# Performance work log

Measured on AMD Instinct MI355X. Metric: run time of the kernel, lower is better.

## Reference

```python
import jax, jax.numpy as jnp
import numpy as np


def _lstm(x, h0, c0, Wih, Whh, b):
    """Single-layer LSTM, batch_first input x: [B,T,D]. PyTorch gate order i,f,g,o.
    Returns (h_seq [T,B,H], h_T [B,H], c_T [B,H])."""
    xs = jnp.swapaxes(x, 0, 1)  # [T,B,D]

    def step(carry, xt):
        h, c = carry
        gates = xt @ Wih.T + h @ Whh.T + b  # [B,4H]
        i, f, g, o = jnp.split(gates, 4, axis=-1)
        c = jax.nn.sigmoid(f) * c + jax.nn.sigmoid(i) * jnp.tanh(g)
        h = jax.nn.sigmoid(o) * jnp.tanh(c)
        return (h, c), h

    (h, c), hs = jax.lax.scan(step, (h0, c0), xs)
    return hs, h, c


def setup_inputs() -> dict:
    key = jax.random.key(0)
    ks = jax.random.split(key, 16)
    B, T, Tf, Tu = 256, 365, 15, 76
    Dh, Df, Du, H = 64, 32, 16, 256
    s = 1.0 / np.sqrt(H)  # torch-style uniform scale, approximated with scaled normals
    return {
        "x_d": jax.random.normal(ks[0], (B, T, Dh), jnp.float32),
        "x_f": jax.random.normal(ks[1], (B, Tf, Df), jnp.float32),
        "x_ff": jax.random.normal(ks[2], (B, Tu, Du), jnp.float32),
        "enc_Wih": jax.random.normal(ks[3], (4 * H, Dh), jnp.float32) * s,
        "enc_Whh": jax.random.normal(ks[4], (4 * H, H), jnp.float32) * s,
        "enc_b": jax.random.normal(ks[5], (4 * H,), jnp.float32) * s,
        "decf_Wih": jax.random.normal(ks[6], (4 * H, Df), jnp.float32) * s,
        "decf_Whh": jax.random.normal(ks[7], (4 * H, H), jnp.float32) * s,
        "decf_b": jax.random.normal(ks[8], (4 * H,), jnp.float32) * s,
        "decu_Wih": jax.random.normal(ks[9], (4 * H, Du), jnp.float32) * s,
        "decu_Whh": jax.random.normal(ks[10], (4 * H, H), jnp.float32) * s,
        "decu_b": jax.random.normal(ks[11], (4 * H,), jnp.float32) * s,
        "head_W": jax.random.normal(ks[12], (1, H), jnp.float32) * s,
        "head_b": jax.random.normal(ks[13], (1,), jnp.float32) * s,
    }


def reference(x_d, x_f, x_ff, enc_Wih, enc_Whh, enc_b,
              decf_Wih, decf_Whh, decf_b, decu_Wih, decu_Whh, decu_b,
              head_W, head_b):
    B = x_d.shape[0]
    H = enc_Whh.shape[1]
    Tf = x_f.shape[1]
    Tu = x_ff.shape[1]
    horizon = Tf + Tu
    h0 = jnp.zeros((B, H), x_d.dtype)
    c0 = jnp.zeros((B, H), x_d.dtype)

    # Encoder over historical sequence
    _, h, c = _lstm(x_d, h0, c0, enc_Wih, enc_Whh, enc_b)

    # Forecast decoder: one LSTM step per horizon step + linear head (dropout = eval identity)
    hs_f, h, c = _lstm(x_f, h, c, decf_Wih, decf_Whh, decf_b)  # [Tf,B,H]
    out_f = (jnp.einsum('tbh,oh->tbo', hs_f, head_W)[..., 0] + head_b[0]).T  # [B,Tf]

    # Future decoder, continuing the hidden state
    hs_u, h, c = _lstm(x_ff, h, c, decu_Wih, decu_Whh, decu_b)  # [Tu,B,H]
    out_u = (jnp.einsum('tbh,oh->tbo', hs_u, head_W)[..., 0] + head_b[0]).T  # [B,Tu]

    # Faithful to original: both loops write outputs[:, t], so the future loop
    # overwrites the first Tu columns.
    outputs = jnp.zeros((B, horizon), x_d.dtype)
    outputs = outputs.at[:, :Tf].set(out_f)
    outputs = outputs.at[:, :Tu].set(out_u)
    return outputs
```

## Files before the change

### kernel.cpp

```cpp
#include <hip/hip_runtime.h>
#include <stdint.h>


typedef __attribute__((ext_vector_type(8))) short short8;
typedef __attribute__((ext_vector_type(4))) float f32x4;
typedef __attribute__((ext_vector_type(2))) unsigned int u32x2;
typedef __attribute__((ext_vector_type(4))) unsigned int u32x4;

#define L2E 1.4426950408889634f

__device__ __forceinline__ uint16_t f2bf(float f) {
  uint32_t x = __float_as_uint(f);
  x += 0x7fffu + ((x >> 16) & 1u);
  return (uint16_t)(x >> 16);
}
__device__ __forceinline__ uint32_t cvtpk(float lo, float hi) {
  uint32_t r;
  asm("v_cvt_pk_bf16_f32 %0, %1, %2" : "=v"(r) : "v"(lo), "v"(hi));
  return r;
}
__device__ __forceinline__ float bfhalf(uint32_t w, int hi) {
  return __uint_as_float(hi ? (w & 0xffff0000u) : (w << 16));
}
__device__ __forceinline__ f32x4 MFMA(short8 a, short8 b, f32x4 c) {
  return __builtin_amdgcn_mfma_f32_16x16x32_bf16(a, b, c, 0, 0, 0);
}
__device__ __forceinline__ float ex2(float x) { return __builtin_amdgcn_exp2f(x); }
__device__ __forceinline__ float rcp(float x) { return __builtin_amdgcn_rcpf(x); }

__device__ __forceinline__ short8 pack8s(const float* s, float sc) {
  float4 q0 = *(const float4*)s, q1 = *(const float4*)(s + 4);
  u32x4 t;
  t[0] = cvtpk(q0.x * sc, q0.y * sc);
  t[1] = cvtpk(q0.z * sc, q0.w * sc);
  t[2] = cvtpk(q1.x * sc, q1.y * sc);
  t[3] = cvtpk(q1.z * sc, q1.w * sc);
  return *(short8*)&t;
}

__device__ __forceinline__ void lgkm_barrier() {
  __builtin_amdgcn_sched_barrier(0);
  asm volatile("s_waitcnt lgkmcnt(0)" ::: "memory");
  __builtin_amdgcn_s_barrier();
  __builtin_amdgcn_sched_barrier(0);
}
__device__ __forceinline__ void vm_drain4() {
  __builtin_amdgcn_sched_barrier(0);
  asm volatile("s_waitcnt vmcnt(4)" ::: "memory");
  __builtin_amdgcn_sched_barrier(0);
}

__global__ void init_kernel(float* c_state, uint16_t* h_state, float* out) {
  int i = blockIdx.x * 256 + threadIdx.x;
  if (i < 65536) { c_state[i] = 0.f; h_state[i] = 0; }
  if (i < 256 * 91) out[i] = 0.f;
}

template <int DIN>
__device__ __forceinline__ void xproj_body(
    const float* __restrict__ x, const float* __restrict__ Wih,
    const float* __restrict__ bias, uint32_t* __restrict__ xp,
    int T, int blk, int tid) {
  const int w = tid >> 6, l = tid & 63;
  const int l16 = l & 15, lg = l >> 4;
  const int tc = blk >> 1;
  const int sub = blk & 1;
  const int t = tc;
  constexpr int KT = (DIN + 31) / 32;

  short8 bfr[8][KT];
  float4 bias4[8];
#pragma unroll
  for (int ni = 0; ni < 8; ++ni) {
    const int n = (w * 8 + ni) * 16 + l16;
    bias4[ni] = *(const float4*)&bias[(w * 8 + ni) * 16 + lg * 4];
#pragma unroll
    for (int kt = 0; kt < KT; ++kt) {
      const int k0 = kt * 32 + lg * 8;
      short8 fr;
#pragma unroll
      for (int e = 0; e < 8; ++e) fr[e] = 0;
      if (k0 + 8 <= DIN) fr = pack8s(Wih + (size_t)n * DIN + k0, 1.f);
      bfr[ni][kt] = fr;
    }
  }

  for (int mi = 0; mi < 8; ++mi) {
    const int btile = sub * 8 + mi;
    const int b = btile * 16 + l16;
    short8 af[KT];
#pragma unroll
    for (int kt = 0; kt < KT; ++kt) {
      const int k0 = kt * 32 + lg * 8;
      short8 fr;
#pragma unroll
      for (int e = 0; e < 8; ++e) fr[e] = 0;
      if (k0 + 8 <= DIN) fr = pack8s(x + ((size_t)b * T + t) * DIN + k0, 1.f);
      af[kt] = fr;
    }
#pragma unroll
    for (int ni = 0; ni < 8; ++ni) {
      f32x4 acc = {0.f, 0.f, 0.f, 0.f};
#pragma unroll
      for (int kt = 0; kt < KT; ++kt) acc = MFMA(bfr[ni][kt], af[kt], acc);
      const int nt = w * 8 + ni;
      const float sc = ((nt >> 4) == 2) ? (2.f * L2E) : -L2E;
      size_t idx = ((((size_t)tc * 16 + btile) * 64 + nt) * 64 + l) * 2;
      u32x2 v;
      v[0] = cvtpk((acc[0] + bias4[ni].x) * sc, (acc[1] + bias4[ni].y) * sc);
      v[1] = cvtpk((acc[2] + bias4[ni].z) * sc, (acc[3] + bias4[ni].w) * sc);
      *(u32x2*)(xp + idx) = v;
    }
  }
}

template <int DIN>
__global__ __launch_bounds__(512) void xproj_kernel(
    const float* __restrict__ x, const float* __restrict__ Wih,
    const float* __restrict__ bias, uint32_t* __restrict__ xp,
    int t0, int T) {
  const int tid = threadIdx.x;
  const int blk = blockIdx.x + t0 * 2;
  xproj_body<DIN>(x, Wih, bias, xp - (size_t)t0 * 131072, T, blk, tid);
}

__global__ __launch_bounds__(512) void xproj_mega(
    const float* __restrict__ x0, const float* __restrict__ Wih0,
    const float* __restrict__ b0, uint32_t* __restrict__ xp0,
    const float* __restrict__ x1, const float* __restrict__ Wih1,
    const float* __restrict__ b1, uint32_t* __restrict__ xp1,
    const float* __restrict__ x2, const float* __restrict__ Wih2,
    const float* __restrict__ b2, uint32_t* __restrict__ xp2,
    float* __restrict__ out, uint32_t* __restrict__ flags,
    int T0, int T1, int T2) {
  const int tid = threadIdx.x;
  const int n0 = T0 * 2, n1 = T1 * 2, n2 = T2 * 2;
  const int b = blockIdx.x;
  if (b < n0) {
    xproj_body<64>(x0, Wih0, b0, xp0, T0, b, tid);
  } else if (b < n0 + n1) {
    xproj_body<32>(x1, Wih1, b1, xp1, T1, b - n0, tid);
  } else if (b < n0 + n1 + n2) {
    xproj_body<16>(x2, Wih2, b2, xp2, T2, b - n0 - n1, tid);
  } else {
    for (int i = tid; i < 256 * 15; i += 512)
      out[(size_t)(i / 15) * 91 + 76 + (i % 15)] = 0.f;
    if (tid < 96) flags[tid] = 0;
  }
}

template <int DO_HEAD, int ZINIT>
__global__ __launch_bounds__(512, 2) void rec_kernel(
    const uint32_t* __restrict__ xp, const float* __restrict__ Whh,
    float* __restrict__ c_state, uint16_t* __restrict__ h_state,
    float* __restrict__ out, const float* __restrict__ headW,
    const float* __restrict__ headb, int ct, int tcol0) {
  __shared__ short8 B_lds[8 * 16 * 64];
  __shared__ uint16_t h_lds[2][16][264];
  __shared__ float headbuf[2][16][8];

  const int tid = threadIdx.x, w = tid >> 6, l = tid & 63;
  const int l16 = l & 15, lg = l >> 4;
  const int blk = blockIdx.x, b0 = blk * 16;

  short8 bv[48];
#pragma unroll
  for (int g = 0; g < 4; ++g) {
    const float wsc = (g == 2) ? (2.f * L2E) : -L2E;
#pragma unroll
    for (int nt = 0; nt < 2; ++nt)
#pragma unroll
      for (int kt = 0; kt < 8; ++kt) {
        const int row = (g * 16 + w * 2 + nt) * 16 + l16;
        const float* s = Whh + (size_t)row * 256 + kt * 32 + lg * 8;
        short8 fr;
#pragma unroll
        for (int e = 0; e < 8; ++e) fr[e] = (short)f2bf(s[e] * wsc);
        const int tile = g * 2 + nt;
        if (kt <= 5) bv[tile * 6 + kt] = fr;
        else B_lds[(w * 16 + (kt - 6) * 8 + tile) * 64 + l] = fr;
      }
  }

  float c_reg[2][4];
  if (ZINIT) {
#pragma unroll
    for (int nt = 0; nt < 2; ++nt)
#pragma unroll
      for (int j = 0; j < 4; ++j) c_reg[nt][j] = 0.f;
    for (int idx = tid; idx < 16 * 264; idx += 512)
      ((uint16_t*)h_lds)[idx] = 0;
  } else {
#pragma unroll
    for (int nt = 0; nt < 2; ++nt) {
      float4 c4 = *(const float4*)&c_state[(size_t)(b0 + l16) * 256 +
                                           (w * 2 + nt) * 16 + lg * 4];
      c_reg[nt][0] = c4.x; c_reg[nt][1] = c4.y;
      c_reg[nt][2] = c4.z; c_reg[nt][3] = c4.w;
    }
    for (int idx = tid; idx < 16 * 256; idx += 512)
      h_lds[0][idx >> 8][idx & 255] = h_state[(size_t)(b0 + (idx >> 8)) * 256 + (idx & 255)];
  }
  float4 hw4[2];
#pragma unroll
  for (int nt = 0; nt < 2; ++nt)
    hw4[nt] = *(const float4*)&headW[(w * 2 + nt) * 16 + lg * 4];
  const float hb = headb[0];

  const uint32_t* xpb = xp + ((size_t)(blk * 64 + w * 2) * 64 + l) * 2;
  u32x2 xpf[2][4];
#pragma unroll
  for (int nt = 0; nt < 2; ++nt)
#pragma unroll
    for (int g = 0; g < 4; ++g)
      xpf[nt][g] = *(const u32x2*)(xpb + (size_t)g * 2048 + nt * 128);

  __syncthreads();

  for (int t = 0; t < ct; ++t) {
    const int cur = t & 1, nxt = cur ^ 1;
    const int tn = (t + 1 < ct) ? t + 1 : t;
    float hp = 0.f;

#pragma unroll
    for (int nt = 0; nt < 2; ++nt) {
      f32x4 acc[4];
#pragma unroll
      for (int g = 0; g < 4; ++g) {
        f32x4 ai;
        ai[0] = bfhalf(xpf[nt][g][0], 0);
        ai[1] = bfhalf(xpf[nt][g][0], 1);
        ai[2] = bfhalf(xpf[nt][g][1], 0);
        ai[3] = bfhalf(xpf[nt][g][1], 1);
        acc[g] = ai;
      }
#pragma unroll
      for (int kt = 0; kt <= 5; ++kt) {
        short8 hf = *(const short8*)(&h_lds[cur][l16][kt * 32 + lg * 8]);
#pragma unroll
        for (int g = 0; g < 4; ++g)
          acc[g] = MFMA(bv[(g * 2 + nt) * 6 + kt], hf, acc[g]);
      }
#pragma unroll
      for (int kt = 6; kt <= 7; ++kt) {
        short8 hf = *(const short8*)(&h_lds[cur][l16][kt * 32 + lg * 8]);
#pragma unroll
        for (int g = 0; g < 4; ++g)
          acc[g] = MFMA(B_lds[(w * 16 + (kt - 6) * 8 + g * 2 + nt) * 64 + l], hf, acc[g]);
      }

      float hv[4];
#pragma unroll
      for (int j = 0; j < 4; ++j) {
        float ei = ex2(acc[0][j]);
        float ef = ex2(acc[1][j]);
        float eg = ex2(acc[2][j]);
        float eo = ex2(acc[3][j]);
        float eip = 1.f + ei, egp = eg + 1.f, efp = 1.f + ef;
        float d1 = eip * egp;
        float R = rcp(d1 * efp);
        float sitg = (eg - 1.f) * efp * R;
        float cc = fmaf(c_reg[nt][j] * d1, R, sitg);
        c_reg[nt][j] = cc;
        float ec = ex2(cc * (2.f * L2E));
        float hh = (ec - 1.f) * rcp((1.f + eo) * (ec + 1.f));
        hv[j] = hh;
      }
      if (DO_HEAD) {
        hp = fmaf(hv[0], hw4[nt].x, hp); hp = fmaf(hv[1], hw4[nt].y, hp);
        hp = fmaf(hv[2], hw4[nt].z, hp); hp = fmaf(hv[3], hw4[nt].w, hp);
      }
      {
        u32x2 hwrd;
        hwrd[0] = cvtpk(hv[0], hv[1]);
        hwrd[1] = cvtpk(hv[2], hv[3]);
        *(u32x2*)(&h_lds[nxt][l16][(w * 2 + nt) * 16 + lg * 4]) = hwrd;
      }
#pragma unroll
      for (int g = 0; g < 4; ++g)
        xpf[nt][g] = *(const u32x2*)(xpb + (size_t)tn * 131072 + g * 2048 + nt * 128);
    }

    if (DO_HEAD) {
      float s = hp;
      s += __shfl_xor(s, 16);
      s += __shfl_xor(s, 32);
      if (lg == 0) headbuf[t & 1][l16][w] = s;
    }

    lgkm_barrier();

    if (DO_HEAD) {
      if (tid < 16) {
        const float* hbp = headbuf[t & 1][tid];
        float s = hbp[0] + hbp[1] + hbp[2] + hbp[3] + hbp[4] + hbp[5] + hbp[6] + hbp[7];
        out[(size_t)(b0 + tid) * 91 + (tcol0 + t)] = s + hb;
      }
    }
  }

#pragma unroll
  for (int nt = 0; nt < 2; ++nt) {
    float4 c4 = {c_reg[nt][0], c_reg[nt][1], c_reg[nt][2], c_reg[nt][3]};
    *(float4*)&c_state[(size_t)(b0 + l16) * 256 + (w * 2 + nt) * 16 + lg * 4] = c4;
  }
  for (int idx = tid; idx < 16 * 256; idx += 512)
    h_state[(size_t)(b0 + (idx >> 8)) * 256 + (idx & 255)] = h_lds[ct & 1][idx >> 8][idx & 255];
}

__global__ __launch_bounds__(512, 2) void rec_split2(
    const uint32_t* __restrict__ xp1g, const uint32_t* __restrict__ xp2g,
    const float* __restrict__ Whh1, const float* __restrict__ Whh2,
    const float* __restrict__ c_state, const uint16_t* __restrict__ h_state,
    float* __restrict__ out, const float* __restrict__ headW,
    const float* __restrict__ headb, uint32_t* __restrict__ flags,
    unsigned long long* __restrict__ hx, uint32_t* __restrict__ hxh,
    int T1, int T2) {
  __shared__ short8 B_lds[64 * 64];
  __shared__ uint16_t h_lds[2][16][264];
  __shared__ float headbuf[16][8];

  const int tid = threadIdx.x, w = tid >> 6, l = tid & 63;
  const int l16 = l & 15, lg = l >> 4;
  const int blk = blockIdx.x;
  const int pair = blk & 15, s = blk >> 4, sp = 1 - s;
  const int b0 = pair * 16;
  const int ctile = s * 8 + w;

  float c_reg[4];
  {
    float4 c4 = *(const float4*)&c_state[(size_t)(b0 + l16) * 256 +
                                         ctile * 16 + lg * 4];
    c_reg[0] = c4.x; c_reg[1] = c4.y; c_reg[2] = c4.z; c_reg[3] = c4.w;
  }
  for (int idx = tid; idx < 16 * 256; idx += 512)
    h_lds[0][idx >> 8][idx & 255] = h_state[(size_t)(b0 + (idx >> 8)) * 256 + (idx & 255)];
  float4 hw4 = *(const float4*)&headW[ctile * 16 + lg * 4];
  const float hb = headb[0];

  float hsum_prev = 0.f;

#pragma unroll
  for (int p = 0; p < 2; ++p) {
    const float* Whh = p ? Whh2 : Whh1;
    const uint32_t* xp = p ? xp2g : xp1g;
    const int ct = p ? T2 : T1;
    const bool headf = (p == 1);
    uint32_t* const pflag = flags + ((1 + p) * 16 + pair) * 2 + sp;
    uint32_t* const myflag = flags + ((1 + p) * 16 + pair) * 2 + s;
    unsigned long long* const hxp = hx + (size_t)p * 32768;
    uint32_t* const hxhp = hxh + p * 1024;

    short8 bv[24];
#pragma unroll
    for (int g = 0; g < 4; ++g) {
      const float wsc = (g == 2) ? (2.f * L2E) : -L2E;
#pragma unroll
      for (int kk = 0; kk < 8; ++kk) {
        const int kt = (kk < 4) ? (4 * s + kk) : (4 * sp + (kk - 4));
        const int row = (g * 16 + ctile) * 16 + l16;
        const float* sw = Whh + (size_t)row * 256 + kt * 32 + lg * 8;
        short8 fr;
#pragma unroll
        for (int e = 0; e < 8; ++e) fr[e] = (short)f2bf(sw[e] * wsc);
        if (kk <= 5) bv[g * 6 + kk] = fr;
        else B_lds[(w * 8 + g * 2 + (kk - 6)) * 64 + l] = fr;
      }
    }

    const uint32_t* xpb = xp + ((size_t)(pair * 64 + ctile) * 64 + l) * 2;
    u32x2 xpf[4];
#pragma unroll
    for (int g = 0; g < 4; ++g)
      xpf[g] = *(const u32x2*)(xpb + (size_t)g * 2048);

    __syncthreads();

    u32x2 h_last; h_last[0] = 0; h_last[1] = 0;

    for (int t = 0; t < ct; ++t) {
      const int cur = t & 1, nxt = cur ^ 1;
      const int tn = (t + 1 < ct) ? t + 1 : t;
      const int par = t & 1;

      unsigned long long pv = 0ull;
      if (t > 0) {
        const uint32_t tgt = (uint32_t)t;
        __builtin_amdgcn_sched_barrier(0);
        uint32_t f;
        do {
          f = __hip_atomic_load(pflag, __ATOMIC_RELAXED, __HIP_MEMORY_SCOPE_AGENT);
        } while ((int)(f - tgt) < 0);
        __builtin_amdgcn_sched_barrier(0);
        pv = __hip_atomic_load(
            hxp + ((size_t)((pair * 2 + sp) * 2 + ((t - 1) & 1)) * 512) +
                (w * 4 + lg) * 16 + l16,
            __ATOMIC_RELAXED, __HIP_MEMORY_SCOPE_AGENT);
        if (headf && s == 0 && tid < 16) {
          uint32_t pp = __hip_atomic_load(
              hxhp + ((pair * 2 + sp) * 2 + ((t - 1) & 1)) * 16 + tid,
              __ATOMIC_RELAXED, __HIP_MEMORY_SCOPE_AGENT);
          out[(size_t)(b0 + tid) * 91 + (t - 1)] =
              hsum_prev + __uint_as_float(pp) + hb;
        }
      }

      f32x4 acc[4];
#pragma unroll
      for (int g = 0; g < 4; ++g) {
        f32x4 ai;
        ai[0] = bfhalf(xpf[g][0], 0);
        ai[1] = bfhalf(xpf[g][0], 1);
        ai[2] = bfhalf(xpf[g][1], 0);
        ai[3] = bfhalf(xpf[g][1], 1);
        acc[g] = ai;
      }
#pragma unroll
      for (int kk = 0; kk < 4; ++kk) {
        short8 hf = *(const short8*)(&h_lds[cur][l16][(4 * s + kk) * 32 + lg * 8]);
#pragma unroll
        for (int g = 0; g < 4; ++g)
          acc[g] = MFMA(bv[g * 6 + kk], hf, acc[g]);
      }

      if (t > 0) {
        u32x2 pw;
        pw[0] = (uint32_t)pv;
        pw[1] = (uint32_t)(pv >> 32);
        *(u32x2*)(&h_lds[cur][l16][sp * 128 + w * 16 + lg * 4]) = pw;
        lgkm_barrier();
      }

#pragma unroll
      for (int kk = 0; kk < 4; ++kk) {
        short8 hf = *(const short8*)(&h_lds[cur][l16][(4 * sp + kk) * 32 + lg * 8]);
#pragma unroll
        for (int g = 0; g < 4; ++g) {
          if (kk < 2) acc[g] = MFMA(bv[g * 6 + 4 + kk], hf, acc[g]);
          else acc[g] = MFMA(B_lds[(w * 8 + g * 2 + (kk - 2)) * 64 + l], hf, acc[g]);
        }
      }

      float hv[4];
#pragma unroll
      for (int j = 0; j < 4; ++j) {
        float ei = ex2(acc[0][j]);
        float ef = ex2(acc[1][j]);
        float eg = ex2(acc[2][j]);
        float eo = ex2(acc[3][j]);
        float eip = 1.f + ei, egp = eg + 1.f, efp = 1.f + ef;
        float d1 = eip * egp;
        float R = rcp(d1 * efp);
        float sitg = (eg - 1.f) * efp * R;
        float cc = fmaf(c_reg[j] * d1, R, sitg);
        c_reg[j] = cc;
        float ec = ex2(cc * (2.f * L2E));
        float hh = (ec - 1.f) * rcp((1.f + eo) * (ec + 1.f));
        hv[j] = hh;
      }

      h_last[0] = cvtpk(hv[0], hv[1]);
      h_last[1] = cvtpk(hv[2], hv[3]);
      *(u32x2*)(&h_lds[nxt][l16][ctile * 16 + lg * 4]) = h_last;
      {
        unsigned long long v64 =
            ((unsigned long long)h_last[1] << 32) | (unsigned long long)h_last[0];
        __hip_atomic_store(
            hxp + ((size_t)((pair * 2 + s) * 2 + par) * 512) + (w * 4 + lg) * 16 + l16,
            v64, __ATOMIC_RELAXED, __HIP_MEMORY_SCOPE_AGENT);
      }

#pragma unroll
      for (int g = 0; g < 4; ++g)
        xpf[g] = *(const u32x2*)(xpb + (size_t)tn * 131072 + g * 2048);

      if (headf) {
        float hp = fmaf(hv[0], hw4.x, fmaf(hv[1], hw4.y,
                   fmaf(hv[2], hw4.z, hv[3] * hw4.w)));
        hp += __shfl_xor(hp, 16);
        hp += __shfl_xor(hp, 32);
        if (lg == 0) headbuf[l16][w] = hp;
      }

      vm_drain4();
      lgkm_barrier();

      if (headf) {
        if (tid < 16) {
          const float* hbp = headbuf[tid];
          hsum_prev = hbp[0] + hbp[1] + hbp[2] + hbp[3] +
                      hbp[4] + hbp[5] + hbp[6] + hbp[7];
          __hip_atomic_store(hxhp + ((pair * 2 + s) * 2 + par) * 16 + tid,
                             __float_as_uint(hsum_prev), __ATOMIC_RELAXED,
                             __HIP_MEMORY_SCOPE_AGENT);
        }
        vm_drain4();
      }
      if (tid == 0)
        __hip_atomic_store(myflag, (uint32_t)(t + 1), __ATOMIC_RELAXED,
                           __HIP_MEMORY_SCOPE_AGENT);
    }

    if (p == 0) {
      const uint32_t tgt = (uint32_t)ct;
      __builtin_amdgcn_sched_barrier(0);
      uint32_t f;
      do {
        f = __hip_atomic_load(pflag, __ATOMIC_RELAXED, __HIP_MEMORY_SCOPE_AGENT);
      } while ((int)(f - tgt) < 0);
      __builtin_amdgcn_sched_barrier(0);
      unsigned long long pv = __hip_atomic_load(
          hxp + ((size_t)((pair * 2 + sp) * 2 + ((ct - 1) & 1)) * 512) +
              (w * 4 + lg) * 16 + l16,
          __ATOMIC_RELAXED, __HIP_MEMORY_SCOPE_AGENT);
      const int fb = ct & 1;
      u32x2 pw;
      pw[0] = (uint32_t)pv;
      pw[1] = (uint32_t)(pv >> 32);
      *(u32x2*)(&h_lds[fb][l16][sp * 128 + w * 16 + lg * 4]) = pw;
      lgkm_barrier();
      if (fb != 0) {
        for (int idx = tid; idx < 1024; idx += 512) {
          const int r = idx >> 6, c4v = (idx & 63) * 4;
          *(u32x2*)(&h_lds[0][r][c4v]) = *(const u32x2*)(&h_lds[1][r][c4v]);
        }
      }
      lgkm_barrier();
    }
  }

  if (s == 0 && tid < 16) {
    uint32_t* const pflag2 = flags + (2 * 16 + pair) * 2 + sp;
    const uint32_t tgt = (uint32_t)T2;
    uint32_t f;
    do {
      f = __hip_atomic_load(pflag2, __ATOMIC_RELAXED, __HIP_MEMORY_SCOPE_AGENT);
    } while ((int)(f - tgt) < 0);
    uint32_t pp = __hip_atomic_load(
        hxh + 1024 + ((pair * 2 + sp) * 2 + ((T2 - 1) & 1)) * 16 + tid,
        __ATOMIC_RELAXED, __HIP_MEMORY_SCOPE_AGENT);
    out[(size_t)(b0 + tid) * 91 + (T2 - 1)] =
        hsum_prev + __uint_as_float(pp) + hb;
  }
}

extern "C" void kernel_launch(void* const* d_in, const int* in_sizes, int n_in,
                              void* d_out, int out_size, void* d_ws, size_t ws_size,
                              hipStream_t stream) {
  const float* headW = (const float*)d_in[12];
  const float* headb = (const float*)d_in[13];
  float* out = (float*)d_out;
  char* ws = (char*)d_ws;

  const int T0 = in_sizes[0] / (256 * 64);
  const int T1 = in_sizes[1] / (256 * 32);
  const int T2 = in_sizes[2] / (256 * 16);
  const size_t s0 = (size_t)T0 << 19, s1 = (size_t)T1 << 19, s2 = (size_t)T2 << 19;
  const size_t hdr = 929792;

  if (ws_size >= hdr + s0 + s1 + s2) {
    float* c_state = (float*)ws;
    uint16_t* h_state = (uint16_t*)(ws + 262144);
    uint32_t* flags = (uint32_t*)(ws + 393216);
    unsigned long long* hx = (unsigned long long*)(ws + 397312);
    uint32_t* hxh = (uint32_t*)(ws + 921600);
    uint32_t* xp0 = (uint32_t*)(ws + hdr);
    uint32_t* xp1 = (uint32_t*)(ws + hdr + s0);
    uint32_t* xp2 = (uint32_t*)(ws + hdr + s0 + s1);

    const int nblk = T0 * 2 + T1 * 2 + T2 * 2 + 1;
    xproj_mega<<<dim3(nblk), 512, 0, stream>>>(
        (const float*)d_in[0], (const float*)d_in[3], (const float*)d_in[5], xp0,
        (const float*)d_in[1], (const float*)d_in[6], (const float*)d_in[8], xp1,
        (const float*)d_in[2], (const float*)d_in[9], (const float*)d_in[11], xp2,
        out, flags, T0, T1, T2);
    rec_kernel<0, 1><<<16, 512, 0, stream>>>(xp0, (const float*)d_in[4], c_state,
                                             h_state, out, headW, headb, T0, 0);
    rec_split2<<<32, 512, 0, stream>>>(xp1, xp2, (const float*)d_in[7],
                                       (const float*)d_in[10], c_state, h_state,
                                       out, headW, headb, flags, hx, hxh, T1, T2);
    return;
  }

  float* c_state = (float*)ws;
  uint16_t* h_state = (uint16_t*)(ws + 262144);
  uint32_t* xp = (uint32_t*)(ws + 393216);

  int ct_max = 1;
  if (ws_size > 393216 + 512 * 1024) {
    size_t c = (ws_size - 393216) / (512 * 1024);
    ct_max = (c > 365) ? 365 : (int)c;
  }

  init_kernel<<<256, 256, 0, stream>>>(c_state, h_state, out);

  struct Phase { const float* x; const float* Wih; const float* Whh; const float* b; int T; int D; int head; };
  Phase ph[3] = {
      {(const float*)d_in[0], (const float*)d_in[3], (const float*)d_in[4], (const float*)d_in[5], T0, 64, 0},
      {(const float*)d_in[1], (const float*)d_in[6], (const float*)d_in[7], (const float*)d_in[8], T1, 32, 0},
      {(const float*)d_in[2], (const float*)d_in[9], (const float*)d_in[10], (const float*)d_in[11], T2, 16, 1},
  };

  for (int pi = 0; pi < 3; ++pi) {
    const Phase& P = ph[pi];
    for (int t0 = 0; t0 < P.T; t0 += ct_max) {
      int ct = (P.T - t0 < ct_max) ? (P.T - t0) : ct_max;
      dim3 g(ct * 2);
      if (P.D == 64)
        xproj_kernel<64><<<g, 512, 0, stream>>>(P.x, P.Wih, P.b, xp, t0, P.T);
      else if (P.D == 32)
        xproj_kernel<32><<<g, 512, 0, stream>>>(P.x, P.Wih, P.b, xp, t0, P.T);
      else
        xproj_kernel<16><<<g, 512, 0, stream>>>(P.x, P.Wih, P.b, xp, t0, P.T);
      if (P.head)
        rec_kernel<1, 0><<<16, 512, 0, stream>>>(xp, P.Whh, c_state, h_state, out,
                                                 headW, headb, ct, t0);
      else
        rec_kernel<0, 0><<<16, 512, 0, stream>>>(xp, P.Whh, c_state, h_state, out,
                                                 headW, headb, ct, t0);
    }
  }
}
```

Before: 1.196 ms.

## Add 1024-thread encoder recurrence kernel holding all Whh fragments in registers

Replaces the 512-thread encoder recurrence kernel with a 1024-thread variant that spreads the 1024 gate columns across 16 waves. Each wave keeps its bf16 Whh fragments in registers (32 short8s instead of 48 plus an LDS buffer), which removes the LDS weight reads from the per-step critical path. It also drops the unused head logic. Doubling the waves per block halves the per-wave serial MFMA chain per timestep, at the cost of a barrier across more waves and higher register pressure per CU.

```diff
diff --git a/kernel.cpp b/kernel.cpp
--- a/kernel.cpp
+++ b/kernel.cpp
@@ -147,6 +147,103 @@
       out[(size_t)(i / 15) * 91 + 76 + (i % 15)] = 0.f;
     if (tid < 96) flags[tid] = 0;
   }
+}
+
+__global__ __launch_bounds__(1024, 4) void rec_enc16(
+    const uint32_t* __restrict__ xp, const float* __restrict__ Whh,
+    float* __restrict__ c_state, uint16_t* __restrict__ h_state, int ct) {
+  __shared__ uint16_t h_lds[2][16][264];
+
+  const int tid = threadIdx.x, w = tid >> 6, l = tid & 63;
+  const int l16 = l & 15, lg = l >> 4;
+  const int blk = blockIdx.x, b0 = blk * 16;
+
+  short8 bv[32];
+#pragma unroll
+  for (int g = 0; g < 4; ++g) {
+    const float wsc = (g == 2) ? (2.f * L2E) : -L2E;
+#pragma unroll
+    for (int kt = 0; kt < 8; ++kt) {
+      const int row = (g * 16 + w) * 16 + l16;
+      const float* s = Whh + (size_t)row * 256 + kt * 32 + lg * 8;
+      short8 fr;
+#pragma unroll
+      for (int e = 0; e < 8; ++e) fr[e] = (short)f2bf(s[e] * wsc);
+      bv[g * 8 + kt] = fr;
+    }
+  }
+
+  float c_reg[4] = {0.f, 0.f, 0.f, 0.f};
+  for (int idx = tid; idx < 16 * 264; idx += 1024)
+    ((uint16_t*)h_lds)[idx] = 0;
+
+  const uint32_t* xpb = xp + ((size_t)blk * 8192) + w * 128 + l * 2;
+  u32x2 xpf[4];
+#pragma unroll
+  for (int g = 0; g < 4; ++g)
+    xpf[g] = *(const u32x2*)(xpb + (size_t)g * 2048);
+
+  __syncthreads();
+
+  for (int t = 0; t < ct; ++t) {
+    const int cur = t & 1, nxt = cur ^ 1;
+    const int tn = (t + 1 < ct) ? t + 1 : t;
+
+    f32x4 acc[4];
+#pragma unroll
+    for (int g = 0; g < 4; ++g) {
+      f32x4 ai;
+      ai[0] = bfhalf(xpf[g][0], 0);
+      ai[1] = bfhalf(xpf[g][0], 1);
+      ai[2] = bfhalf(xpf[g][1], 0);
+      ai[3] = bfhalf(xpf[g][1], 1);
+      acc[g] = ai;
+    }
+#pragma unroll
+    for (int kt = 0; kt < 8; ++kt) {
+      short8 hf = *(const short8*)(&h_lds[cur][l16][kt * 32 + lg * 8]);
+#pragma unroll
+      for (int g = 0; g < 4; ++g)
+        acc[g] = MFMA(bv[g * 8 + kt], hf, acc[g]);
+    }
+
+    float hv[4];
+#pragma unroll
+    for (int j = 0; j < 4; ++j) {
+      float ei = ex2(acc[0][j]);
+      float ef = ex2(acc[1][j]);
+      float eg = ex2(acc[2][j]);
+      float eo = ex2(acc[3][j]);
+      float eip = 1.f + ei, egp = eg + 1.f, efp = 1.f + ef;
+      float d1 = eip * egp;
+      float R = rcp(d1 * efp);
+      float sitg = (eg - 1.f) * efp * R;
+      float cc = fmaf(c_reg[j] * d1, R, sitg);
+      c_reg[j] = cc;
+      float ec = ex2(cc * (2.f * L2E));
+      float hh = (ec - 1.f) * rcp((1.f + eo) * (ec + 1.f));
+      hv[j] = hh;
+    }
+    {
+      u32x2 hwrd;
+      hwrd[0] = cvtpk(hv[0], hv[1]);
+      hwrd[1] = cvtpk(hv[2], hv[3]);
+      *(u32x2*)(&h_lds[nxt][l16][w * 16 + lg * 4]) = hwrd;
+    }
+#pragma unroll
+    for (int g = 0; g < 4; ++g)
+      xpf[g] = *(const u32x2*)(xpb + (size_t)tn * 131072 + g * 2048);
+
+    lgkm_barrier();
+  }
+
+  {
+    float4 c4 = {c_reg[0], c_reg[1], c_reg[2], c_reg[3]};
+    *(float4*)&c_state[(size_t)(b0 + l16) * 256 + w * 16 + lg * 4] = c4;
+  }
+  for (int idx = tid; idx < 16 * 256; idx += 1024)
+    h_state[(size_t)(b0 + (idx >> 8)) * 256 + (idx & 255)] =
+        h_lds[ct & 1][idx >> 8][idx & 255];
 }
 
 template <int DO_HEAD, int ZINIT>
@@ -574,8 +671,8 @@
         (const float*)d_in[1], (const float*)d_in[6], (const float*)d_in[8], xp1,
         (const float*)d_in[2], (const float*)d_in[9], (const float*)d_in[11], xp2,
         out, flags, T0, T1, T2);
-    rec_kernel<0, 1><<<16, 512, 0, stream>>>(xp0, (const float*)d_in[4], c_state,
-                                             h_state, out, headW, headb, T0, 0);
+    rec_enc16<<<16, 1024, 0, stream>>>(xp0, (const float*)d_in[4], c_state,
+                                       h_state, T0);
     rec_split2<<<32, 512, 0, stream>>>(xp1, xp2, (const float*)d_in[7],
                                        (const float*)d_in[10], c_state, h_state,
                                        out, headW, headb, flags, hx, hxh, T1, T2);
```

New measurement: 2.442 ms. +104.2%, slower.
